# Optimization experiments

Measured on AMD Instinct MI355X. Metric: run time of the kernel, lower is better.

Reference implementation:

```python
import jax, jax.numpy as jnp
from jax import lax
import numpy as np

DN = ('NCHW', 'OIHW', 'NCHW')

def conv(x, w, b, stride, pad):
    y = lax.conv_general_dilated(x, w, (stride, stride), [(pad, pad), (pad, pad)], dimension_numbers=DN)
    return y if b is None else y + b[None, :, None, None]

def conv_transpose(x, w, b):
    # torch ConvTranspose2d(k=4, s=2, p=1); w in torch layout (Cin, Cout, 4, 4)
    w_f = jnp.flip(w, (2, 3)).transpose(1, 0, 2, 3)  # -> OIHW, flipped
    y = lax.conv_general_dilated(x, w_f, (1, 1), [(2, 2), (2, 2)], lhs_dilation=(2, 2), dimension_numbers=DN)
    return y + b[None, :, None, None]

def res_stack(x, w3, w1, n_layers=2):
    # shared weights across layers (ModuleList([layer]*n) aliases one module)
    for _ in range(n_layers):
        h = conv(jax.nn.relu(x), w3, None, 1, 1)
        h = conv(jax.nn.relu(h), w1, None, 1, 0)
        x = x + h
    return jax.nn.relu(x)

def setup_inputs() -> dict:
    key = jax.random.key(0)
    ks = jax.random.split(key, 16)
    s = 0.02
    d = {
        'x': jax.random.normal(ks[0], (32, 3, 256, 256), jnp.float32),
        'enc_w1': jax.random.normal(ks[1], (128, 3, 4, 4), jnp.float32) * s,
        'enc_b1': jnp.zeros((128,), jnp.float32),
        'enc_w2': jax.random.normal(ks[2], (256, 128, 4, 4), jnp.float32) * s,
        'enc_b2': jnp.zeros((256,), jnp.float32),
        'enc_w3': jax.random.normal(ks[3], (512, 256, 4, 4), jnp.float32) * s,
        'enc_b3': jnp.zeros((512,), jnp.float32),
        'enc_res_w3': jax.random.normal(ks[4], (32, 512, 3, 3), jnp.float32) * s,
        'enc_res_w1': jax.random.normal(ks[5], (512, 32, 1, 1), jnp.float32) * s,
        'prevq_w': jax.random.normal(ks[6], (64, 512, 1, 1), jnp.float32) * s,
        'prevq_b': jnp.zeros((64,), jnp.float32),
        'emb': jax.random.normal(ks[7], (512, 64), jnp.float32),
        'dec_w1': jax.random.normal(ks[8], (64, 256, 4, 4), jnp.float32) * s,
        'dec_b1': jnp.zeros((256,), jnp.float32),
        'dec_res_w3': jax.random.normal(ks[9], (32, 256, 3, 3), jnp.float32) * s,
        'dec_res_w1': jax.random.normal(ks[10], (256, 32, 1, 1), jnp.float32) * s,
        'dec_w2': jax.random.normal(ks[11], (256, 128, 4, 4), jnp.float32) * s,
        'dec_b2': jnp.zeros((128,), jnp.float32),
        'dec_w3': jax.random.normal(ks[12], (128, 3, 4, 4), jnp.float32) * s,
        'dec_b3': jnp.zeros((3,), jnp.float32),
    }
    return d

def vqvae_fwd(x, enc_w1, enc_b1, enc_w2, enc_b2, enc_w3, enc_b3, enc_res_w3, enc_res_w1,
              prevq_w, prevq_b, emb, dec_w1, dec_b1, dec_res_w3, dec_res_w1,
              dec_w2, dec_b2, dec_w3, dec_b3):
    # encoder
    z = jax.nn.relu(conv(x, enc_w1, enc_b1, 2, 1))
    z = jax.nn.relu(conv(z, enc_w2, enc_b2, 2, 1))
    z = conv(z, enc_w3, enc_b3, 2, 1)
    z = res_stack(z, enc_res_w3, enc_res_w1)
    z_e = conv(z, prevq_w, prevq_b, 1, 0)  # (B, D=64, 32, 32)
    # vector quantiser
    B, C, H, W = z_e.shape
    x_flat = z_e.reshape(B, C, H * W).transpose(0, 2, 1)  # (B, HW, D)
    d2 = (jnp.sum(x_flat ** 2, -1, keepdims=True)
          - 2.0 * jnp.einsum('bnd,kd->bnk', x_flat, emb)
          + jnp.sum(emb ** 2, -1))
    idx = jnp.argmin(d2, axis=2)  # (B, HW)
    z_q_flat = emb[idx]  # (B, HW, D)
    z_q = z_q_flat.transpose(0, 2, 1).reshape(B, C, H, W)
    sg = lax.stop_gradient
    q_loss = jnp.mean((sg(z_q_flat) - x_flat) ** 2) + jnp.mean((z_q_flat - sg(x_flat)) ** 2)
    # decoder
    y = conv_transpose(z_q, dec_w1, dec_b1)  # (B, 256, 64, 64)
    y = res_stack(y, dec_res_w3, dec_res_w1)
    y = jax.nn.relu(conv_transpose(y, dec_w2, dec_b2))
    y = conv_transpose(y, dec_w3, dec_b3)  # (B, 3, 256, 256)
    return y, q_loss

def reference(x, enc_w1, enc_b1, enc_w2, enc_b2, enc_w3, enc_b3, enc_res_w3, enc_res_w1,
              prevq_w, prevq_b, emb, dec_w1, dec_b1, dec_res_w3, dec_res_w1,
              dec_w2, dec_b2, dec_w3, dec_b3):
    return vqvae_fwd(x, enc_w1, enc_b1, enc_w2, enc_b2, enc_w3, enc_b3, enc_res_w3, enc_res_w1,
                     prevq_w, prevq_b, emb, dec_w1, dec_b1, dec_res_w3, dec_res_w1,
                     dec_w2, dec_b2, dec_w3, dec_b3)
```

## Files before the change

kernel.cpp:

```cpp
#include <hip/hip_runtime.h>
#include <hip/hip_bf16.h>

typedef __attribute__((ext_vector_type(8))) short short8;
typedef __attribute__((ext_vector_type(4))) float f32x4;
typedef __attribute__((ext_vector_type(4))) unsigned int uint4v;

__device__ __forceinline__ unsigned short f2bf(float f) {
  unsigned u = __builtin_bit_cast(unsigned, f);
  u = (u + 0x7FFFu + ((u >> 16) & 1u)) >> 16;
  return (unsigned short)u;
}
__device__ __forceinline__ float bf2f(unsigned short h) {
  unsigned u = ((unsigned)h) << 16;
  return __builtin_bit_cast(float, u);
}
__device__ __forceinline__ unsigned pk_bf16(float a, float b) {
  __hip_bfloat162 h = __float22bfloat162_rn(make_float2(a, b));
  unsigned u;
  __builtin_memcpy(&u, &h, 4);
  return u;
}

template<int TMT, int MT, int MODE, int ZSP, bool SPLIT, bool RELU_IN, bool RELU_OUT, bool BIAS, int SM>
__global__ __launch_bounds__(256, 4) void k_mfconv(
    const float* __restrict__ in, const unsigned short* __restrict__ wp,
    const float* __restrict__ bias, float* __restrict__ out,
    int Ci, int inW, int inH, int pWSH, int pHWSH,
    int Co, int ntap, int ntt,
    unsigned syp, unsigned sxp,
    int outW, int outHW, int CoSt) {
  const int tid  = threadIdx.x;
  const int lane = tid & 63, wave = tid >> 6;
  const int pW  = 1 << pWSH;
  const int pHW = 1 << pHWSH;
  const int inHW = inW * inH;
  const int nk32 = Ci >> 5;
  const int KS   = (nk32 >= 2) ? 2 : 1;
  const int NITS = 4 * KS;
  const int cpt  = nk32 / KS;
  const int total = ntap * cpt;
  constexpr int TT = TMT * MT;

  int bx = blockIdx.x;
  const int gx = gridDim.x;
  if ((gx & 7) == 0) bx = (bx & 7) * (gx >> 3) + (bx >> 3);
  const int n0  = bx * 64;
  const int coG = blockIdx.y;
  const int ph  = (MODE == 1) ? blockIdx.z : 0;
  const int tap0 = (MODE == 1) ? ph * 4 : 0;
  const int pdy = ph >> 1, pdx = ph & 1;

  int it0 = 0, itEnd = total;
  if (MODE != 1 && ZSP > 1) {
    const int per = total / ZSP;
    it0 = blockIdx.z * per;
    itEnd = it0 + per;
  }

  constexpr int NPL = SPLIT ? 2 : 1;
  constexpr int PL = 64 * 70;
  __shared__ __align__(16) unsigned short Bs[2 * NPL * PL];

  const int px  = lane;
  const int p   = n0 + px;
  const int img = p >> pHWSH;
  const int rem = p & (pHW - 1);
  const int y   = rem >> pWSH;
  const int x   = rem & (pW - 1);
  const size_t base_img = (size_t)img * Ci * inHW;

  constexpr int NTO = (TMT == 4) ? 4 : 2;
  const int mt0 = (TMT == 4) ? wave : (wave & 1);
  const int ntb = (TMT == 4) ? 0 : ((wave >> 1) * 2);
  f32x4 acc[MT * NTO];
#pragma unroll
  for (int u = 0; u < MT * NTO; ++u) acc[u] = (f32x4){0.f, 0.f, 0.f, 0.f};

  const int cp = wave;
  float v[16];

  auto ldr = [&](int tap_, int chunk_) {
    const int T = tap0 + tap_;
    const int dy = (int)((syp >> (2 * T)) & 3u) - 1;
    const int dx = (int)((sxp >> (2 * T)) & 3u) - 1;
    const int ys = (MODE == 2) ? (2 * y + dy) : (y + dy);
    const int xs = (MODE == 2) ? (2 * x + dx) : (x + dx);
    const bool ok = ((unsigned)ys < (unsigned)inH) && ((unsigned)xs < (unsigned)inW);
    const float* __restrict__ ipb = in + base_img + (ptrdiff_t)ys * inW + xs;
    const int ci0 = chunk_ * (KS * 32);
#pragma unroll
    for (int it2 = 0; it2 < 8; ++it2) {
      if (it2 >= NITS) break;
      const int cl = 2 * (cp + 4 * it2);
      float a = 0.f, b = 0.f;
      if (ok) {
        a = ipb[(size_t)(ci0 + cl) * inHW];
        b = ipb[(size_t)(ci0 + cl + 1) * inHW];
      }
      if (RELU_IN) { a = fmaxf(a, 0.f); b = fmaxf(b, 0.f); }
      v[2 * it2] = a; v[2 * it2 + 1] = b;
    }
  };
  auto pwr = [&](int b) {
#pragma unroll
    for (int it2 = 0; it2 < 8; ++it2) {
      if (it2 >= NITS) break;
      const int cl = 2 * (cp + 4 * it2);
      float a = v[2 * it2], c = v[2 * it2 + 1];
      unsigned hp = pk_bf16(a, c);
      *(unsigned*)&Bs[(b * NPL) * PL + px * 70 + cl] = hp;
      if (SPLIT) {
        float h0 = bf2f((unsigned short)hp), h1 = bf2f((unsigned short)(hp >> 16));
        *(unsigned*)&Bs[(b * NPL + 1) * PL + px * 70 + cl] = pk_bf16(a - h0, c - h1);
      }
    }
  };

  int tap = it0 / cpt, chunk = it0 % cpt;
  ldr(tap, chunk);
  pwr(0);
  __syncthreads();

  for (int it = it0; it < itEnd; ++it) {
    const int b = (it - it0) & 1;
    const int T = tap0 + tap;
    int tap2 = tap, chunk2 = chunk + 1;
    if (chunk2 == cpt) { chunk2 = 0; tap2 = tap + 1; }
    const bool more = (it + 1 < itEnd);
    if (more) ldr(tap2, chunk2);
#pragma unroll
    for (int s = 0; s < 2; ++s) {
      if (s >= KS) break;
      const int cic = chunk * KS + s;
      short8 ah[MT], al[MT];
#pragma unroll
      for (int m = 0; m < MT; ++m) {
        const int mtm = mt0 + m * TMT;
        size_t abase;
        if (SPLIT) abase = ((((size_t)coG * ntt + T) * nk32 + cic) * 2 * TT + mtm) * 512;
        else       abase = ((((size_t)coG * ntt + T) * nk32 + cic) * TT + mtm) * 512;
        ah[m] = *(const short8*)(wp + abase + (size_t)lane * 8);
        if (SPLIT) al[m] = *(const short8*)(wp + abase + (size_t)TT * 512 + (size_t)lane * 8);
      }
      short8 bh[NTO], bl[NTO];
#pragma unroll
      for (int u = 0; u < NTO; ++u) {
        const int row = 16 * (ntb + u) + (lane & 15);
        const unsigned* bp = (const unsigned*)&Bs[(b * NPL) * PL + row * 70 + s * 32 + (lane >> 4) * 8];
        uint4v hv = {bp[0], bp[1], bp[2], bp[3]};
        bh[u] = __builtin_bit_cast(short8, hv);
        if (SPLIT) {
          const unsigned* bpl = bp + (PL >> 1);
          uint4v lv = {bpl[0], bpl[1], bpl[2], bpl[3]};
          bl[u] = __builtin_bit_cast(short8, lv);
        }
      }
#pragma unroll
      for (int m = 0; m < MT; ++m)
#pragma unroll
        for (int u = 0; u < NTO; ++u) {
          f32x4 a = acc[m * NTO + u];
          a = __builtin_amdgcn_mfma_f32_16x16x32_bf16(ah[m], bh[u], a, 0, 0, 0);
          if (SPLIT) {
            a = __builtin_amdgcn_mfma_f32_16x16x32_bf16(al[m], bh[u], a, 0, 0, 0);
            a = __builtin_amdgcn_mfma_f32_16x16x32_bf16(ah[m], bl[u], a, 0, 0, 0);
          }
          acc[m * NTO + u] = a;
        }
    }
    if (more) {
      pwr(b ^ 1);
      __syncthreads();
    }
    tap = tap2; chunk = chunk2;
  }

#pragma unroll
  for (int m = 0; m < MT; ++m) {
    const int mtm = mt0 + m * TMT;
#pragma unroll
    for (int u = 0; u < NTO; ++u) {
      const int nt = ntb + u;
      const int pn = n0 + nt * 16 + (lane & 15);
      const int img2 = pn >> pHWSH;
      const int rem2 = pn & (pHW - 1);
      const int y2 = rem2 >> pWSH, x2 = rem2 & (pW - 1);
      int oy, ox;
      if (MODE == 1) { oy = 2 * y2 + pdy; ox = 2 * x2 + pdx; }
      else           { oy = y2;           ox = x2; }
#pragma unroll
      for (int r = 0; r < 4; ++r) {
        const int co = coG * (TT * 16) + mtm * 16 + (lane >> 4) * 4 + r;
        if (co < CoSt) {
          float val = acc[m * NTO + u][r];
          if (BIAS) val += bias[co];
          if (RELU_OUT) val = fmaxf(val, 0.f);
          size_t oi = ((size_t)img2 * Co + co) * outHW + (size_t)oy * outW + ox;
          if (SM == 0) out[oi] = val;
          else if (SM == 1) out[oi] += val;
          else atomicAdd(&out[oi], val);
        }
      }
    }
  }
}

__global__ __launch_bounds__(256, 4) void k_mfenc1(
    const float* __restrict__ in, const unsigned short* __restrict__ wp,
    const float* __restrict__ bias, float* __restrict__ out) {
  const int tid = threadIdx.x, lane = tid & 63, wave = tid >> 6;
  int bx = blockIdx.x;
  const int gx = gridDim.x;
  if ((gx & 7) == 0) bx = (bx & 7) * (gx >> 3) + (bx >> 3);
  const int n0 = bx * 64;
  const int p = n0 + lane;
  const int img = p >> 14;
  const int rem = p & 16383;
  const int y = rem >> 7, x = rem & 127;
  __shared__ __align__(16) unsigned short Bs[2 * 4480];
  const float* __restrict__ ib = in + (size_t)img * 3 * 65536;
#pragma unroll
  for (int i = 0; i < 8; ++i) {
    const int kk0 = 2 * (wave + 4 * i);
    float vv[2];
#pragma unroll
    for (int q = 0; q < 2; ++q) {
      const int kk = kk0 + q;
      const int tap = kk >> 2, c = kk & 3;
      const int iy = 2 * y + (tap >> 2) - 1, ix = 2 * x + (tap & 3) - 1;
      const bool ok = (c < 3) && ((unsigned)iy < 256u) && ((unsigned)ix < 256u);
      vv[q] = ok ? ib[((size_t)c << 16) + (size_t)iy * 256 + ix] : 0.f;
    }
    unsigned hp = pk_bf16(vv[0], vv[1]);
    *(unsigned*)&Bs[lane * 70 + kk0] = hp;
    float h0 = bf2f((unsigned short)hp), h1 = bf2f((unsigned short)(hp >> 16));
    *(unsigned*)&Bs[4480 + lane * 70 + kk0] = pk_bf16(vv[0] - h0, vv[1] - h1);
  }
  __syncthreads();

  f32x4 acc[8];
#pragma unroll
  for (int u = 0; u < 8; ++u) acc[u] = (f32x4){0.f, 0.f, 0.f, 0.f};
#pragma unroll
  for (int s = 0; s < 2; ++s) {
    short8 ah[2], al[2];
#pragma unroll
    for (int m = 0; m < 2; ++m) {
      const int mtm = wave + m * 4;
      size_t abase = (((size_t)s * 2 + 0) * 8 + mtm) * 512;
      ah[m] = *(const short8*)(wp + abase + (size_t)lane * 8);
      al[m] = *(const short8*)(wp + abase + 8 * 512 + (size_t)lane * 8);
    }
    short8 bh[4], bl[4];
#pragma unroll
    for (int u = 0; u < 4; ++u) {
      const int row = 16 * u + (lane & 15);
      const unsigned* bp = (const unsigned*)&Bs[row * 70 + s * 32 + (lane >> 4) * 8];
      uint4v hv = {bp[0], bp[1], bp[2], bp[3]};
      bh[u] = __builtin_bit_cast(short8, hv);
      const unsigned* bpl = bp + 2240;
      uint4v lv = {bpl[0], bpl[1], bpl[2], bpl[3]};
      bl[u] = __builtin_bit_cast(short8, lv);
    }
#pragma unroll
    for (int m = 0; m < 2; ++m)
#pragma unroll
      for (int u = 0; u < 4; ++u) {
        f32x4 a = acc[m * 4 + u];
        a = __builtin_amdgcn_mfma_f32_16x16x32_bf16(ah[m], bh[u], a, 0, 0, 0);
        a = __builtin_amdgcn_mfma_f32_16x16x32_bf16(al[m], bh[u], a, 0, 0, 0);
        a = __builtin_amdgcn_mfma_f32_16x16x32_bf16(ah[m], bl[u], a, 0, 0, 0);
        acc[m * 4 + u] = a;
      }
  }
#pragma unroll
  for (int m = 0; m < 2; ++m)
#pragma unroll
    for (int u = 0; u < 4; ++u) {
      const int pn = n0 + u * 16 + (lane & 15);
      const int img2 = pn >> 14;
      const int rem2 = pn & 16383;
#pragma unroll
      for (int r = 0; r < 4; ++r) {
        const int co = (wave + m * 4) * 16 + (lane >> 4) * 4 + r;
// ... 314 lines not shown
      e2  = fmaf(ev, ev, e2);
    }
    float score = e2 - 2.f * dot;
    if (score < best) { best = score; bi = k; }
  }
  const float* __restrict__ eb = emb + (size_t)bi * 64;
  float* __restrict__ qp = zq + (size_t)n * 64 * P + p;
  float l = 0.f;
#pragma unroll
  for (int d = 0; d < 64; ++d) {
    float ev = eb[d];
    qp[(size_t)d * P] = ev;
    float df = ev - xv[d];
    l = fmaf(df, df, l);
  }
#pragma unroll
  for (int off = 32; off > 0; off >>= 1) l += __shfl_down(l, off, 64);
  if ((threadIdx.x & 63) == 0) atomicAdd(loss, l * (2.f / 2097152.f));
}

extern "C" void kernel_launch(void* const* d_in, const int* in_sizes, int n_in,
                              void* d_out, int out_size, void* d_ws, size_t ws_size,
                              hipStream_t stream) {
  const float* x    = (const float*)d_in[0];
  const float* ew1  = (const float*)d_in[1];
  const float* eb1  = (const float*)d_in[2];
  const float* ew2  = (const float*)d_in[3];
  const float* eb2  = (const float*)d_in[4];
  const float* ew3  = (const float*)d_in[5];
  const float* eb3  = (const float*)d_in[6];
  const float* erw3 = (const float*)d_in[7];
  const float* erw1 = (const float*)d_in[8];
  const float* pqw  = (const float*)d_in[9];
  const float* pqb  = (const float*)d_in[10];
  const float* emb  = (const float*)d_in[11];
  const float* dw1  = (const float*)d_in[12];
  const float* db1  = (const float*)d_in[13];
  const float* drw3 = (const float*)d_in[14];
  const float* drw1 = (const float*)d_in[15];
  const float* dw2  = (const float*)d_in[16];
  const float* db2  = (const float*)d_in[17];
  const float* dw3  = (const float*)d_in[18];
  const float* db3  = (const float*)d_in[19];
  float* out = (float*)d_out;
  char*  ws  = (char*)d_ws;
  float* loss = out + 6291456;
  const size_t MiB = 1048576ull, KiB = 1024ull;

  dim3 blk(256);
  hipMemsetAsync(loss, 0, 4, stream);

  unsigned syct = 0, sxct = 0;
  for (int T = 0; T < 16; ++T) {
    int phx = T >> 2, dy = phx >> 1, dx = phx & 1, t = T & 3, ty = t >> 1, tx = t & 1;
    int sy = (dy == 0) ? (ty ? -1 : 0) : (ty ? 0 : 1);
    int sx = (dx == 0) ? (tx ? -1 : 0) : (tx ? 0 : 1);
    syct |= (unsigned)(sy + 1) << (2 * T);
    sxct |= (unsigned)(sx + 1) << (2 * T);
  }
  unsigned syc3 = 0, sxc3 = 0;
  for (int t = 0; t < 9; ++t) {
    syc3 |= (unsigned)(t / 3) << (2 * t);
    sxc3 |= (unsigned)(t % 3) << (2 * t);
  }
  unsigned syc4 = 0, sxc4 = 0;
  for (int t = 0; t < 16; ++t) {
    syc4 |= (unsigned)(t / 4) << (2 * t);
    sxc4 |= (unsigned)(t % 4) << (2 * t);
  }
  const unsigned sy1 = 1, sx1 = 1;

  auto packs = [&](char* PB) {
    unsigned short* e2p   = (unsigned short*)(PB);
    unsigned short* e3p   = (unsigned short*)(PB + 2048 * KiB);
    unsigned short* erc3p = (unsigned short*)(PB + 10240 * KiB);
    unsigned short* erc1p = (unsigned short*)(PB + 10816 * KiB);
    unsigned short* pqp   = (unsigned short*)(PB + 10880 * KiB);
    unsigned short* d1p   = (unsigned short*)(PB + 11008 * KiB);
    unsigned short* d2p   = (unsigned short*)(PB + 11520 * KiB);
    unsigned short* dc3p  = (unsigned short*)(PB + 12544 * KiB);
    unsigned short* dc1p  = (unsigned short*)(PB + 12688 * KiB);
    unsigned short* e1p   = (unsigned short*)(PB + 12704 * KiB);
    unsigned short* d3p   = (unsigned short*)(PB + 12832 * KiB);
    k_pack_o<true ><<<dim3(1048576 / 256), blk, 0, stream>>>(ew2,  e2p,  256, 128, 16, 8, 1048576);
    k_pack_o<true ><<<dim3(4194304 / 256), blk, 0, stream>>>(ew3,  e3p,  512, 256, 16, 8, 4194304);
    k_pack_o<true ><<<dim3(294912 / 256),  blk, 0, stream>>>(erw3, erc3p, 32, 512,  9, 2, 294912);
    k_pack_o<true ><<<dim3(32768 / 256),   blk, 0, stream>>>(erw1, erc1p, 512, 32,  1, 8, 32768);
    k_pack_o<true ><<<dim3(65536 / 256),   blk, 0, stream>>>(pqw,  pqp,   64, 512,  1, 4, 65536);
    k_pack_ct<<<dim3(262144 / 256), blk, 0, stream>>>(dw1, d1p, 64, 256, 8, 262144);
    k_pack_ct<<<dim3(524288 / 256), blk, 0, stream>>>(dw2, d2p, 256, 128, 8, 524288);
    k_pack_o<false><<<dim3(73728 / 256),   blk, 0, stream>>>(drw3, dc3p,  32, 256,  9, 2, 73728);
    k_pack_o<false><<<dim3(8192 / 256),    blk, 0, stream>>>(drw1, dc1p, 256, 32,  1, 8, 8192);
    k_pack_e1<<<dim3(256), blk, 0, stream>>>(ew1, e1p);
    k_pack_ct<<<dim3(65536 / 256), blk, 0, stream>>>(dw3, d3p, 128, 3, 2, 65536);
  };

  if (ws_size >= 498ull * MiB) {
    float* z1 = (float*)ws;
    float* z2 = (float*)(ws + 256 * MiB);
    float* z3 = (float*)(ws + 384 * MiB);
    float* h  = (float*)(ws + 448 * MiB);
    float* ze = (float*)(ws + 452 * MiB);
    float* zq = (float*)(ws + 460 * MiB);
    float* hd = (float*)(ws + 468 * MiB);
    char*  PB = ws + 484 * MiB;
    unsigned short* e2p   = (unsigned short*)(PB);
    unsigned short* e3p   = (unsigned short*)(PB + 2048 * KiB);
    unsigned short* erc3p = (unsigned short*)(PB + 10240 * KiB);
    unsigned short* erc1p = (unsigned short*)(PB + 10816 * KiB);
    unsigned short* pqp   = (unsigned short*)(PB + 10880 * KiB);
    unsigned short* d1p   = (unsigned short*)(PB + 11008 * KiB);
    unsigned short* d2p   = (unsigned short*)(PB + 11520 * KiB);
    unsigned short* dc3p  = (unsigned short*)(PB + 12544 * KiB);
    unsigned short* dc1p  = (unsigned short*)(PB + 12688 * KiB);
    unsigned short* e1p   = (unsigned short*)(PB + 12704 * KiB);
    unsigned short* d3p   = (unsigned short*)(PB + 12832 * KiB);
    packs(PB);

    k_mfenc1<<<dim3(8192), blk, 0, stream>>>(x, e1p, eb1, z1);
    k_mfconv<4, 2, 2, 1, true, false, true, true, 0><<<dim3(2048, 2), blk, 0, stream>>>(
        z1, e2p, eb2, z2, 128, 128, 128, 6, 12, 256, 16, 16, syc4, sxc4, 64, 4096, 256);
    k_mfconv<4, 2, 2, 1, true, false, false, true, 0><<<dim3(512, 4), blk, 0, stream>>>(
        z2, e3p, eb3, z3, 256, 64, 64, 5, 10, 512, 16, 16, syc4, sxc4, 32, 1024, 512);
    for (int i = 0; i < 2; ++i) {
      hipMemsetAsync(h, 0, 4 * MiB, stream);
      k_mfconv<2, 1, 0, 3, true, true, false, false, 2><<<dim3(512, 1, 3), blk, 0, stream>>>(
          z3, erc3p, nullptr, h, 512, 32, 32, 5, 10, 32, 9, 9, syc3, sxc3, 32, 1024, 32);
      k_mfconv<4, 2, 0, 1, true, true, false, false, 1><<<dim3(512, 4), blk, 0, stream>>>(
          h, erc1p, nullptr, z3, 32, 32, 32, 5, 10, 512, 1, 1, sy1, sx1, 32, 1024, 512);
    }
    hipMemsetAsync(ze, 0, 8 * MiB, stream);
    k_mfconv<4, 1, 0, 4, true, true, false, false, 2><<<dim3(512, 1, 4), blk, 0, stream>>>(
        z3, pqp, nullptr, ze, 512, 32, 32, 5, 10, 64, 1, 1, sy1, sx1, 32, 1024, 64);
    k_vq<<<dim3(128), blk, 0, stream>>>(ze, emb, pqb, zq, loss);
    float* y1 = (float*)(ws + 256 * MiB);
    float* y2 = (float*)ws;
    k_mfconv<4, 2, 1, 1, false, false, false, true, 0><<<dim3(512, 2, 4), blk, 0, stream>>>(
        zq, d1p, db1, y1, 64, 32, 32, 5, 10, 256, 4, 16, syct, sxct, 64, 4096, 256);
    for (int i = 0; i < 2; ++i) {
      hipMemsetAsync(hd, 0, 16 * MiB, stream);
      k_mfconv<2, 1, 0, 3, false, true, false, false, 2><<<dim3(2048, 1, 3), blk, 0, stream>>>(
          y1, dc3p, nullptr, hd, 256, 64, 64, 6, 12, 32, 9, 9, syc3, sxc3, 64, 4096, 32);
      k_mfconv<4, 2, 0, 1, false, true, false, false, 1><<<dim3(2048, 2), blk, 0, stream>>>(
          hd, dc1p, nullptr, y1, 32, 64, 64, 6, 12, 256, 1, 1, sy1, sx1, 64, 4096, 256);
    }
    k_mfconv<4, 2, 1, 1, false, true, true, true, 0><<<dim3(2048, 1, 4), blk, 0, stream>>>(
        y1, d2p, db2, y2, 256, 64, 64, 6, 12, 128, 4, 16, syct, sxct, 128, 16384, 128);
    k_mfconv<2, 1, 1, 1, false, false, false, true, 0><<<dim3(8192, 1, 4), blk, 0, stream>>>(
        y2, d3p, db3, out, 128, 128, 128, 7, 14, 3, 4, 16, syct, sxct, 256, 65536, 3);
    return;
  }

  if (ws_size >= 128ull * MiB) {
    float* z3  = (float*)ws;
    float* h   = (float*)(ws + 64 * MiB);
    float* ze  = (float*)(ws + 68 * MiB);
    float* zq  = (float*)(ws + 100 * MiB);
    char*  PB  = ws + 115 * MiB;
    unsigned short* e2p   = (unsigned short*)(PB);
    unsigned short* e3p   = (unsigned short*)(PB + 2048 * KiB);
    unsigned short* erc3p = (unsigned short*)(PB + 10240 * KiB);
    unsigned short* erc1p = (unsigned short*)(PB + 10816 * KiB);
    unsigned short* pqp   = (unsigned short*)(PB + 10880 * KiB);
    unsigned short* d1p   = (unsigned short*)(PB + 11008 * KiB);
    unsigned short* d2p   = (unsigned short*)(PB + 11520 * KiB);
    unsigned short* dc3p  = (unsigned short*)(PB + 12544 * KiB);
    unsigned short* dc1p  = (unsigned short*)(PB + 12688 * KiB);
    unsigned short* e1p   = (unsigned short*)(PB + 12704 * KiB);
    unsigned short* d3p   = (unsigned short*)(PB + 12832 * KiB);
    packs(PB);

    const int NE = 4;
    float* z1c = (float*)(ws + 64 * MiB);
    float* z2c = (float*)(ws + 96 * MiB);
    for (int n0 = 0; n0 < 32; n0 += NE) {
      const float* xb = x + (size_t)n0 * 3 * 65536;
      float* z3b = z3 + (size_t)n0 * 512 * 1024;
      k_mfenc1<<<dim3(NE * 256), blk, 0, stream>>>(xb, e1p, eb1, z1c);
      k_mfconv<4, 2, 2, 1, true, false, true, true, 0><<<dim3(256, 2), blk, 0, stream>>>(
          z1c, e2p, eb2, z2c, 128, 128, 128, 6, 12, 256, 16, 16, syc4, sxc4, 64, 4096, 256);
      k_mfconv<4, 2, 2, 1, true, false, false, true, 0><<<dim3(64, 4), blk, 0, stream>>>(
          z2c, e3p, eb3, z3b, 256, 64, 64, 5, 10, 512, 16, 16, syc4, sxc4, 32, 1024, 512);
    }
    for (int i = 0; i < 2; ++i) {
      hipMemsetAsync(h, 0, 4 * MiB, stream);
      k_mfconv<2, 1, 0, 3, true, true, false, false, 2><<<dim3(512, 1, 3), blk, 0, stream>>>(
          z3, erc3p, nullptr, h, 512, 32, 32, 5, 10, 32, 9, 9, syc3, sxc3, 32, 1024, 32);
      k_mfconv<4, 2, 0, 1, true, true, false, false, 1><<<dim3(512, 4), blk, 0, stream>>>(
          h, erc1p, nullptr, z3, 32, 32, 32, 5, 10, 512, 1, 1, sy1, sx1, 32, 1024, 512);
    }
    hipMemsetAsync(ze, 0, 8 * MiB, stream);
    k_mfconv<4, 1, 0, 4, true, true, false, false, 2><<<dim3(512, 1, 4), blk, 0, stream>>>(
        z3, pqp, nullptr, ze, 512, 32, 32, 5, 10, 64, 1, 1, sy1, sx1, 32, 1024, 64);
    k_vq<<<dim3(128), blk, 0, stream>>>(ze, emb, pqb, zq, loss);

    const int ND = 8;
    float* y1c = (float*)ws;
    float* hd  = (float*)(ws + 32 * MiB);
    float* y2c = (float*)(ws + 36 * MiB);
    for (int c = 0; c < 32; c += ND) {
      const float* zqb = zq + (size_t)c * 64 * 1024;
      float* outb = out + (size_t)c * 3 * 65536;
      k_mfconv<4, 2, 1, 1, false, false, false, true, 0><<<dim3(128, 2, 4), blk, 0, stream>>>(
          zqb, d1p, db1, y1c, 64, 32, 32, 5, 10, 256, 4, 16, syct, sxct, 64, 4096, 256);
      for (int i = 0; i < 2; ++i) {
        hipMemsetAsync(hd, 0, 4 * MiB, stream);
        k_mfconv<2, 1, 0, 3, false, true, false, false, 2><<<dim3(512, 1, 3), blk, 0, stream>>>(
            y1c, dc3p, nullptr, hd, 256, 64, 64, 6, 12, 32, 9, 9, syc3, sxc3, 64, 4096, 32);
        k_mfconv<4, 2, 0, 1, false, true, false, false, 1><<<dim3(512, 2), blk, 0, stream>>>(
            hd, dc1p, nullptr, y1c, 32, 64, 64, 6, 12, 256, 1, 1, sy1, sx1, 64, 4096, 256);
      }
      k_mfconv<4, 2, 1, 1, false, true, true, true, 0><<<dim3(512, 1, 4), blk, 0, stream>>>(
          y1c, d2p, db2, y2c, 256, 64, 64, 6, 12, 128, 4, 16, syct, sxct, 128, 16384, 128);
      k_mfconv<2, 1, 1, 1, false, false, false, true, 0><<<dim3(2048, 1, 4), blk, 0, stream>>>(
          y2c, d3p, db3, outb, 128, 128, 128, 7, 14, 3, 4, 16, syct, sxct, 256, 65536, 3);
    }
    return;
  }

  const size_t PER_IMG = 12582912ull;
  int NB = (int)(ws_size / PER_IMG);
  if (NB > 32) NB = 32;
  if (NB < 1)  NB = 1;

  for (int n0 = 0; n0 < 32; n0 += NB) {
    const int nb = (32 - n0 < NB) ? (32 - n0) : NB;
    const float* xb   = x   + (size_t)n0 * 3 * 65536;
    float*       outb = out + (size_t)n0 * 3 * 65536;

    float* z1 = (float*)ws;
    float* z2 = (float*)(ws + (size_t)NB * 8388608ull);
    float* z3 = (float*)ws;
    char*  tb = ws + (size_t)NB * 2097152ull;
    float* he = (float*)tb;
    float* ze = (float*)(tb + (size_t)NB * 131072ull);
    float* zq = (float*)(tb + (size_t)NB * 393216ull);
    float* hd = (float*)(tb + (size_t)NB * 655360ull);
    float* y1 = z2;
    float* y2 = (float*)ws;

    k_conv4<4, true ><<<dim3(8, 8, nb * 32), blk, 0, stream>>>(xb, ew1, eb1, z1, nb,   3, 256, 256, 128);
    k_conv4<4, true ><<<dim3(4, 4, nb * 64), blk, 0, stream>>>(z1, ew2, eb2, z2, nb, 128, 128, 128, 256);
    k_conv4<4, false><<<dim3(2, 2, nb * 128), blk, 0, stream>>>(z2, ew3, eb3, z3, nb, 256,  64,  64, 512);
    for (int i = 0; i < 2; ++i) {
      k_conv3<4, true, 1><<<dim3(2, 2, nb * 8), blk, 0, stream>>>(z3, erw3, he, nb, 512, 32, 32, 32);
      k_conv1<8, true, true><<<dim3(4, 64, nb), blk, 0, stream>>>(he, erw1, nullptr, z3, nb, 32, 1024, 512);
    }
    k_conv1<8, true, false><<<dim3(4, 8, nb), blk, 0, stream>>>(z3, pqw, pqb, ze, nb, 512, 1024, 64);
    k_vq64<<<dim3(nb * 16), dim3(64), 0, stream>>>(ze, emb, zq, loss, nb, 1024, 512);
    k_convT<4, false, false><<<dim3(2, 2, nb * 64), blk, 0, stream>>>(zq, dw1, db1, y1, nb,  64, 32, 32, 256);
    for (int i = 0; i < 2; ++i) {
      k_conv3<4, true, 1><<<dim3(4, 4, nb * 8), blk, 0, stream>>>(y1, drw3, hd, nb, 256, 64, 64, 32);
      k_conv1<8, true, true><<<dim3(16, 32, nb), blk, 0, stream>>>(hd, drw1, nullptr, y1, nb, 32, 4096, 256);
    }
    k_convT<4, true, true ><<<dim3(4, 4, nb * 32), blk, 0, stream>>>(y1, dw2, db2, y2, nb, 256, 64, 64, 128);
    k_convT<1, false, false><<<dim3(8, 8, nb * 3), blk, 0, stream>>>(y2, dw3, db3, outb, nb, 128, 128, 128, 3);
  }
}
```

Baseline: 4.172 ms.

## Add halo-tiled LDS conv kernel for 3x3 and transposed convs, drop split-K atomics

Adds a new kernel, k_mfhalo, that stages a spatial halo tile of 32 input channels in LDS once per channel chunk. All taps (9 for the 3x3, 16 for the transposed conv, covering all four output phases) read their MFMA B operands from that tile instead of re-gathering inputs from global memory per tap. The 3x3 residual convs no longer use split-K with atomicAdd and a preceding memset, and the transposed convs no longer launch one block per phase. The transposed-conv weight packing grouping changes to match. In exchange there is more LDS per block, no double buffering, and a larger accumulator per block for the transposed-conv path, which can lower occupancy.

```diff
diff --git a/kernel.cpp b/kernel.cpp
--- a/kernel.cpp
+++ b/kernel.cpp
@@ -19,6 +19,135 @@
   unsigned u;
   __builtin_memcpy(&u, &h, 4);
   return u;
+}
+
+template<int TMT, int CT, bool SPLIT, bool RELU_IN, bool RELU_OUT, bool BIAS>
+__global__ __launch_bounds__(256, (CT == 1) ? 2 : 4) void k_mfhalo(
+    const float* __restrict__ in, const unsigned short* __restrict__ wp,
+    const float* __restrict__ bias, float* __restrict__ out,
+    int Ci, int inW, int inH, int pWSH, int pHWSH,
+    int Co, int ntt, unsigned syp, unsigned sxp, int CoSt) {
+  constexpr int NTAP = (CT == 1) ? 16 : 9;
+  constexpr int NPH  = (CT == 1) ? 4 : 1;
+  constexpr int NTO  = (TMT == 4) ? 4 : 2;
+  constexpr int PLH  = 224 * 42;
+  const int tid = threadIdx.x, lane = tid & 63, wave = tid >> 6;
+
+  int bx = blockIdx.x;
+  const int gx = gridDim.x;
+  if ((gx & 7) == 0) bx = (bx & 7) * (gx >> 3) + (bx >> 3);
+  const int n0  = bx * 64;
+  const int coG = blockIdx.y;
+
+  const int pW  = 1 << pWSH;
+  const int pHW = 1 << pHWSH;
+  const int W = inW, H = inH;
+  const int inHW = W * H;
+  const int img  = n0 >> pHWSH;
+  const int rem0 = n0 & (pHW - 1);
+  const int y0   = rem0 >> pWSH;
+  const int x0   = rem0 & (pW - 1);
+  const int NR   = (pWSH >= 6) ? 1 : 2;
+  const int HWd  = ((pW < 64) ? pW : 64) + 2;
+  const int HROWS = (NR + 2) * HWd;
+  const int nk32 = Ci >> 5;
+  const size_t base_img = (size_t)img * Ci * inHW;
+
+  __shared__ __align__(16) unsigned short Hs[(SPLIT ? 2 : 1) * PLH];
+
+  const int mt  = (TMT == 4) ? wave : (wave & 1);
+  const int ntb = (TMT == 4) ? 0 : ((wave >> 1) * 2);
+  const int lsh = (pW < 64) ? pWSH : 6;
+  const int lxm = (pW < 64) ? (pW - 1) : 63;
+
+  f32x4 acc[NPH * NTO];
+#pragma unroll
+  for (int u = 0; u < NPH * NTO; ++u) acc[u] = (f32x4){0.f, 0.f, 0.f, 0.f};
+
+  const int srow0 = tid >> 4;
+  const int scl   = (tid & 15) * 2;
+
+  for (int cic = 0; cic < nk32; ++cic) {
+    if (cic) __syncthreads();
+    {
+      const int ci0 = cic * 32;
+      int hy = 0, hx = srow0;
+      for (int h = srow0; h < HROWS; h += 16) {
+        const int iy = y0 - 1 + hy;
+        const int ix = x0 - 1 + hx;
+        const bool ok = ((unsigned)iy < (unsigned)H) && ((unsigned)ix < (unsigned)W);
+        float a = 0.f, b = 0.f;
+        if (ok) {
+          const float* q = in + base_img + (size_t)(ci0 + scl) * inHW + (size_t)iy * W + ix;
+          a = q[0]; b = q[inHW];
+        }
+        if (RELU_IN) { a = fmaxf(a, 0.f); b = fmaxf(b, 0.f); }
+        unsigned hp = pk_bf16(a, b);
+        *(unsigned*)&Hs[h * 42 + scl] = hp;
+        if (SPLIT) {
+          float h0 = bf2f((unsigned short)hp), h1 = bf2f((unsigned short)(hp >> 16));
+          *(unsigned*)&Hs[PLH + h * 42 + scl] = pk_bf16(a - h0, b - h1);
+        }
+        hx += 16; if (hx >= HWd) { hx -= HWd; hy++; }
+      }
+    }
+    __syncthreads();
+#pragma unroll
+    for (int T = 0; T < NTAP; ++T) {
+      const int ency = (int)((syp >> (2 * T)) & 3u);
+      const int encx = (int)((sxp >> (2 * T)) & 3u);
+      size_t abase = (((size_t)coG * ntt + T) * nk32 + cic) * (SPLIT ? 2 : 1) * TMT * 512
+                     + (size_t)mt * 512;
+      short8 ah = *(const short8*)(wp + abase + (size_t)lane * 8);
+      short8 al;
+      if (SPLIT) al = *(const short8*)(wp + abase + (size_t)TMT * 512 + (size_t)lane * 8);
+      const int ph = (CT == 1) ? (T >> 2) : 0;
+#pragma unroll
+      for (int u = 0; u < NTO; ++u) {
+        const int pnl = (ntb + u) * 16 + (lane & 15);
+        const int ly = pnl >> lsh, lx = pnl & lxm;
+        const int h = (ly + ency) * HWd + lx + encx;
+        const unsigned* bp = (const unsigned*)&Hs[h * 42 + (lane >> 4) * 8];
+        uint4v hv = {bp[0], bp[1], bp[2], bp[3]};
+        short8 bh = __builtin_bit_cast(short8, hv);
+        f32x4 a = acc[ph * NTO + u];
+        a = __builtin_amdgcn_mfma_f32_16x16x32_bf16(ah, bh, a, 0, 0, 0);
+        if (SPLIT) {
+          const unsigned* bpl = bp + (PLH >> 1);
+          uint4v lv = {bpl[0], bpl[1], bpl[2], bpl[3]};
+          short8 bl = __builtin_bit_cast(short8, lv);
+          a = __builtin_amdgcn_mfma_f32_16x16x32_bf16(al, bh, a, 0, 0, 0);
+          a = __builtin_amdgcn_mfma_f32_16x16x32_bf16(ah, bl, a, 0, 0, 0);
+        }
+        acc[ph * NTO + u] = a;
+      }
+    }
+  }
+
+  const int outW  = (CT == 1) ? 2 * pW : pW;
+  const int outHW = (CT == 1) ? 4 * pHW : pHW;
+#pragma unroll
+  for (int u = 0; u < NTO; ++u) {
+    const int pn = n0 + (ntb + u) * 16 + (lane & 15);
+    const int rem2 = pn & (pHW - 1);
+    const int y2 = rem2 >> pWSH, x2 = rem2 & (pW - 1);
+#pragma unroll
+    for (int ph = 0; ph < NPH; ++ph) {
+      int oy, ox;
+      if (CT == 1) { oy = 2 * y2 + (ph >> 1); ox = 2 * x2 + (ph & 1); }
+      else         { oy = y2;                 ox = x2; }
+#pragma unroll
+      for (int r = 0; r < 4; ++r) {
+        const int co = coG * (TMT * 16) + mt * 16 + (lane >> 4) * 4 + r;
+        if (co < CoSt) {
+          float val = acc[ph * NTO + u][r];
+          if (BIAS) val += bias[co];
+          if (RELU_OUT) val = fmaxf(val, 0.f);
+          out[((size_t)img * Co + co) * outHW + (size_t)oy * outW + ox] = val;
+        }
+      }
+    }
+  }
 }
 
 template<int TMT, int MT, int MODE, int ZSP, bool SPLIT, bool RELU_IN, bool RELU_OUT, bool BIAS, int SM>
@@ -46,12 +175,9 @@
   if ((gx & 7) == 0) bx = (bx & 7) * (gx >> 3) + (bx >> 3);
   const int n0  = bx * 64;
   const int coG = blockIdx.y;
-  const int ph  = (MODE == 1) ? blockIdx.z : 0;
-  const int tap0 = (MODE == 1) ? ph * 4 : 0;
-  const int pdy = ph >> 1, pdx = ph & 1;
 
   int it0 = 0, itEnd = total;
-  if (MODE != 1 && ZSP > 1) {
+  if (ZSP > 1) {
     const int per = total / ZSP;
     it0 = blockIdx.z * per;
     itEnd = it0 + per;
@@ -80,7 +206,7 @@
   float v[16];
 
   auto ldr = [&](int tap_, int chunk_) {
-    const int T = tap0 + tap_;
+    const int T = tap_;
     const int dy = (int)((syp >> (2 * T)) & 3u) - 1;
     const int dx = (int)((sxp >> (2 * T)) & 3u) - 1;
     const int ys = (MODE == 2) ? (2 * y + dy) : (y + dy);
@@ -123,7 +249,7 @@
 
   for (int it = it0; it < itEnd; ++it) {
     const int b = (it - it0) & 1;
-    const int T = tap0 + tap;
+    const int T = tap;
     int tap2 = tap, chunk2 = chunk + 1;
     if (chunk2 == cpt) { chunk2 = 0; tap2 = tap + 1; }
     const bool more = (it + 1 < itEnd);
@@ -185,9 +311,6 @@
       const int img2 = pn >> pHWSH;
       const int rem2 = pn & (pHW - 1);
       const int y2 = rem2 >> pWSH, x2 = rem2 & (pW - 1);
-      int oy, ox;
-      if (MODE == 1) { oy = 2 * y2 + pdy; ox = 2 * x2 + pdx; }
-      else           { oy = y2;           ox = x2; }
 #pragma unroll
       for (int r = 0; r < 4; ++r) {
         const int co = coG * (TT * 16) + mtm * 16 + (lane >> 4) * 4 + r;
@@ -195,7 +318,7 @@
           float val = acc[m * NTO + u][r];
           if (BIAS) val += bias[co];
           if (RELU_OUT) val = fmaxf(val, 0.f);
-          size_t oi = ((size_t)img2 * Co + co) * outHW + (size_t)oy * outW + ox;
+          size_t oi = ((size_t)img2 * Co + co) * outHW + (size_t)y2 * outW + x2;
           if (SM == 0) out[oi] = val;
           else if (SM == 1) out[oi] += val;
           else atomicAdd(&out[oi], val);
@@ -685,8 +808,8 @@
     k_pack_o<true ><<<dim3(294912 / 256),  blk, 0, stream>>>(erw3, erc3p, 32, 512,  9, 2, 294912);
     k_pack_o<true ><<<dim3(32768 / 256),   blk, 0, stream>>>(erw1, erc1p, 512, 32,  1, 8, 32768);
     k_pack_o<true ><<<dim3(65536 / 256),   blk, 0, stream>>>(pqw,  pqp,   64, 512,  1, 4, 65536);
-    k_pack_ct<<<dim3(262144 / 256), blk, 0, stream>>>(dw1, d1p, 64, 256, 8, 262144);
-    k_pack_ct<<<dim3(524288 / 256), blk, 0, stream>>>(dw2, d2p, 256, 128, 8, 524288);
+    k_pack_ct<<<dim3(262144 / 256), blk, 0, stream>>>(dw1, d1p, 64, 256, 4, 262144);
+    k_pack_ct<<<dim3(524288 / 256), blk, 0, stream>>>(dw2, d2p, 256, 128, 4, 524288);
     k_pack_o<false><<<dim3(73728 / 256),   blk, 0, stream>>>(drw3, dc3p,  32, 256,  9, 2, 73728);
     k_pack_o<false><<<dim3(8192 / 256),    blk, 0, stream>>>(drw1, dc1p, 256, 32,  1, 8, 8192);
     k_pack_e1<<<dim3(256), blk, 0, stream>>>(ew1, e1p);
@@ -721,9 +844,8 @@
     k_mfconv<4, 2, 2, 1, true, false, false, true, 0><<<dim3(512, 4), blk, 0, stream>>>(
         z2, e3p, eb3, z3, 256, 64, 64, 5, 10, 512, 16, 16, syc4, sxc4, 32, 1024, 512);
     for (int i = 0; i < 2; ++i) {
-      hipMemsetAsync(h, 0, 4 * MiB, stream);
-      k_mfconv<2, 1, 0, 3, true, true, false, false, 2><<<dim3(512, 1, 3), blk, 0, stream>>>(
-          z3, erc3p, nullptr, h, 512, 32, 32, 5, 10, 32, 9, 9, syc3, sxc3, 32, 1024, 32);
+      k_mfhalo<2, 0, true, true, false, false><<<dim3(512, 1), blk, 0, stream>>>(
+          z3, erc3p, nullptr, h, 512, 32, 32, 5, 10, 32, 9, syc3, sxc3, 32);
       k_mfconv<4, 2, 0, 1, true, true, false, false, 1><<<dim3(512, 4), blk, 0, stream>>>(
           h, erc1p, nullptr, z3, 32, 32, 32, 5, 10, 512, 1, 1, sy1, sx1, 32, 1024, 512);
     }
@@ -733,19 +855,18 @@
     k_vq<<<dim3(128), blk, 0, stream>>>(ze, emb, pqb, zq, loss);
     float* y1 = (float*)(ws + 256 * MiB);
     float* y2 = (float*)ws;
-    k_mfconv<4, 2, 1, 1, false, false, false, true, 0><<<dim3(512, 2, 4), blk, 0, stream>>>(
-        zq, d1p, db1, y1, 64, 32, 32, 5, 10, 256, 4, 16, syct, sxct, 64, 4096, 256);
+    k_mfhalo<4, 1, false, false, false, true><<<dim3(512, 4), blk, 0, stream>>>(
+        zq, d1p, db1, y1, 64, 32, 32, 5, 10, 256, 16, syct, sxct, 256);
     for (int i = 0; i < 2; ++i) {
-      hipMemsetAsync(hd, 0, 16 * MiB, stream);
-      k_mfconv<2, 1, 0, 3, false, true, false, false, 2><<<dim3(2048, 1, 3), blk, 0, stream>>>(
-          y1, dc3p, nullptr, hd, 256, 64, 64, 6, 12, 32, 9, 9, syc3, sxc3, 64, 4096, 32);
+      k_mfhalo<2, 0, false, true, false, false><<<dim3(2048, 1), blk, 0, stream>>>(
+          y1, dc3p, nullptr, hd, 256, 64, 64, 6, 12, 32, 9, syc3, sxc3, 32);
       k_mfconv<4, 2, 0, 1, false, true, false, false, 1><<<dim3(2048, 2), blk, 0, stream>>>(
           hd, dc1p, nullptr, y1, 32, 64, 64, 6, 12, 256, 1, 1, sy1, sx1, 64, 4096, 256);
     }
-    k_mfconv<4, 2, 1, 1, false, true, true, true, 0><<<dim3(2048, 1, 4), blk, 0, stream>>>(
-        y1, d2p, db2, y2, 256, 64, 64, 6, 12, 128, 4, 16, syct, sxct, 128, 16384, 128);
-    k_mfconv<2, 1, 1, 1, false, false, false, true, 0><<<dim3(8192, 1, 4), blk, 0, stream>>>(
-        y2, d3p, db3, out, 128, 128, 128, 7, 14, 3, 4, 16, syct, sxct, 256, 65536, 3);
+    k_mfhalo<4, 1, false, true, true, true><<<dim3(2048, 2), blk, 0, stream>>>(
+        y1, d2p, db2, y2, 256, 64, 64, 6, 12, 128, 16, syct, sxct, 128);
+    k_mfhalo<2, 1, false, false, false, true><<<dim3(8192, 1), blk, 0, stream>>>(
+        y2, d3p, db3, out, 128, 128, 128, 7, 14, 3, 16, syct, sxct, 3);
     return;
   }
 
@@ -781,9 +902,8 @@
           z2c, e3p, eb3, z3b, 256, 64, 64, 5, 10, 512, 16, 16, syc4, sxc4, 32, 1024, 512);
     }
     for (int i = 0; i < 2; ++i) {
-      hipMemsetAsync(h, 0, 4 * MiB, stream);
-      k_mfconv<2, 1, 0, 3, true, true, false, false, 2><<<dim3(512, 1, 3), blk, 0, stream>>>(
-          z3, erc3p, nullptr, h, 512, 32, 32, 5, 10, 32, 9, 9, syc3, sxc3, 32, 1024, 32);
+      k_mfhalo<2, 0, true, true, false, false><<<dim3(512, 1), blk, 0, stream>>>(
+          z3, erc3p, nullptr, h, 512, 32, 32, 5, 10, 32, 9, syc3, sxc3, 32);
       k_mfconv<4, 2, 0, 1, true, true, false, false, 1><<<dim3(512, 4), blk, 0, stream>>>(
           h, erc1p, nullptr, z3, 32, 32, 32, 5, 10, 512, 1, 1, sy1, sx1, 32, 1024, 512);
     }
@@ -799,19 +919,18 @@
     for (int c = 0; c < 32; c += ND) {
       const float* zqb = zq + (size_t)c * 64 * 1024;
       float* outb = out + (size_t)c * 3 * 65536;
-      k_mfconv<4, 2, 1, 1, false, false, false, true, 0><<<dim3(128, 2, 4), blk, 0, stream>>>(
-          zqb, d1p, db1, y1c, 64, 32, 32, 5, 10, 256, 4, 16, syct, sxct, 64, 4096, 256);
+      k_mfhalo<4, 1, false, false, false, true><<<dim3(128, 4), blk, 0, stream>>>(
+          zqb, d1p, db1, y1c, 64, 32, 32, 5, 10, 256, 16, syct, sxct, 256);
       for (int i = 0; i < 2; ++i) {
-        hipMemsetAsync(hd, 0, 4 * MiB, stream);
-        k_mfconv<2, 1, 0, 3, false, true, false, false, 2><<<dim3(512, 1, 3), blk, 0, stream>>>(
-            y1c, dc3p, nullptr, hd, 256, 64, 64, 6, 12, 32, 9, 9, syc3, sxc3, 64, 4096, 32);
+        k_mfhalo<2, 0, false, true, false, false><<<dim3(512, 1), blk, 0, stream>>>(
+            y1c, dc3p, nullptr, hd, 256, 64, 64, 6, 12, 32, 9, syc3, sxc3, 32);
         k_mfconv<4, 2, 0, 1, false, true, false, false, 1><<<dim3(512, 2), blk, 0, stream>>>(
             hd, dc1p, nullptr, y1c, 32, 64, 64, 6, 12, 256, 1, 1, sy1, sx1, 64, 4096, 256);
       }
-      k_mfconv<4, 2, 1, 1, false, true, true, true, 0><<<dim3(512, 1, 4), blk, 0, stream>>>(
-          y1c, d2p, db2, y2c, 256, 64, 64, 6, 12, 128, 4, 16, syct, sxct, 128, 16384, 128);
-      k_mfconv<2, 1, 1, 1, false, false, false, true, 0><<<dim3(2048, 1, 4), blk, 0, stream>>>(
-          y2c, d3p, db3, outb, 128, 128, 128, 7, 14, 3, 4, 16, syct, sxct, 256, 65536, 3);
+      k_mfhalo<4, 1, false, true, true, true><<<dim3(512, 2), blk, 0, stream>>>(
+          y1c, d2p, db2, y2c, 256, 64, 64, 6, 12, 128, 16, syct, sxct, 128);
+      k_mfhalo<2, 1, false, false, false, true><<<dim3(2048, 1), blk, 0, stream>>>(
+          y2c, d3p, db3, outb, 128, 128, 128, 7, 14, 3, 16, syct, sxct, 3);
     }
     return;
   }
```

After: 4.240 ms. Within noise of the previous version (+1.6%).

## Fuse residual 3x3 and 1x1 convolutions into one kernel per layer

Applied to the files above, without the earlier changes.

Adds k_mfres, which computes relu->3x3 conv (to 32 channels)->relu->1x1 conv->residual add in a single kernel. The hidden activation stays in shared memory instead of global memory, which removes the memset, the split-K atomic adds and the separate 1x1 pass. The kernel ping-pongs between two buffers so it does not write in place. In exchange, each block now covers all 9 taps and all input channels serially, which lowers parallelism compared with the split-K launches. It also needs new weight packings and adds shared-memory pressure.

```diff
diff --git a/kernel.cpp b/kernel.cpp
--- a/kernel.cpp
+++ b/kernel.cpp
@@ -200,6 +200,173 @@
           else if (SM == 1) out[oi] += val;
           else atomicAdd(&out[oi], val);
         }
+      }
+    }
+  }
+}
+
+template<int MGRP, bool SPLIT>
+__global__ __launch_bounds__(256, SPLIT ? 3 : 4) void k_mfres(
+    const float* __restrict__ in, const unsigned short* __restrict__ w3p,
+    const unsigned short* __restrict__ w1p, float* __restrict__ znew,
+    int pWSH, int pHWSH, unsigned syp, unsigned sxp) {
+  constexpr int C = MGRP * 64;
+  const int tid = threadIdx.x, lane = tid & 63, wave = tid >> 6;
+  const int pW = 1 << pWSH, pHW = 1 << pHWSH;
+  const int inW = pW, inH = pHW >> pWSH;
+  const int inHW = pHW;
+  const int nk32 = C >> 5;
+  const int cpt = nk32 >> 1;
+  const int total = 9 * cpt;
+
+  int bx = blockIdx.x;
+  const int gx = gridDim.x;
+  if ((gx & 7) == 0) bx = (bx & 7) * (gx >> 3) + (bx >> 3);
+  const int n0 = bx * 64;
+
+  constexpr int NPL = SPLIT ? 2 : 1;
+  constexpr int PL = 64 * 70;
+  __shared__ __align__(16) unsigned short Bs[2 * NPL * PL];
+  __shared__ __align__(16) unsigned short Hs2[NPL * 2560];
+
+  const int px = lane;
+  const int p = n0 + px;
+  const int img = p >> pHWSH;
+  const int rem = p & (pHW - 1);
+  const int y = rem >> pWSH, x = rem & (pW - 1);
+  const size_t base_img = (size_t)img * C * inHW;
+  const int mt = wave & 1, ntb = (wave >> 1) * 2;
+  const int cp = wave;
+  float v[16];
+  f32x4 acc[2];
+  acc[0] = (f32x4){0.f, 0.f, 0.f, 0.f};
+  acc[1] = (f32x4){0.f, 0.f, 0.f, 0.f};
+
+  auto ldr = [&](int T, int chunk_) {
+    const int dy = (int)((syp >> (2 * T)) & 3u) - 1;
+    const int dx = (int)((sxp >> (2 * T)) & 3u) - 1;
+    const int ys = y + dy, xs = x + dx;
+    const bool ok = ((unsigned)ys < (unsigned)inH) && ((unsigned)xs < (unsigned)inW);
+    const float* __restrict__ ipb = in + base_img + (ptrdiff_t)ys * inW + xs;
+    const int ci0 = chunk_ * 64;
+#pragma unroll
+    for (int i2 = 0; i2 < 8; ++i2) {
+      const int cl = 2 * (cp + 4 * i2);
+      float a = 0.f, b = 0.f;
+      if (ok) {
+        a = ipb[(size_t)(ci0 + cl) * inHW];
+        b = ipb[(size_t)(ci0 + cl + 1) * inHW];
+      }
+      a = fmaxf(a, 0.f); b = fmaxf(b, 0.f);
+      v[2 * i2] = a; v[2 * i2 + 1] = b;
+    }
+  };
+  auto pwr = [&](int b) {
+#pragma unroll
+    for (int i2 = 0; i2 < 8; ++i2) {
+      const int cl = 2 * (cp + 4 * i2);
+      float a = v[2 * i2], c = v[2 * i2 + 1];
+      unsigned hp = pk_bf16(a, c);
+      *(unsigned*)&Bs[(b * NPL) * PL + px * 70 + cl] = hp;
+      if (SPLIT) {
+        float h0 = bf2f((unsigned short)hp), h1 = bf2f((unsigned short)(hp >> 16));
+        *(unsigned*)&Bs[(b * NPL + 1) * PL + px * 70 + cl] = pk_bf16(a - h0, c - h1);
+      }
+    }
+  };
+
+  int tap = 0, chunk = 0;
+  ldr(0, 0);
+  pwr(0);
+  __syncthreads();
+  for (int it = 0; it < total; ++it) {
+    const int b = it & 1;
+    const int T = tap;
+    int tap2 = tap, chunk2 = chunk + 1;
+    if (chunk2 == cpt) { chunk2 = 0; tap2 = tap + 1; }
+    const bool more = (it + 1 < total);
+    if (more) ldr(tap2, chunk2);
+#pragma unroll
+    for (int s = 0; s < 2; ++s) {
+      const int cic = chunk * 2 + s;
+      size_t abase;
+      if (SPLIT) abase = (((size_t)T * nk32 + cic) * 2 * 2 + mt) * 512;
+      else       abase = (((size_t)T * nk32 + cic) * 2 + mt) * 512;
+      short8 ah = *(const short8*)(w3p + abase + (size_t)lane * 8);
+      short8 al;
+      if (SPLIT) al = *(const short8*)(w3p + abase + 2 * 512 + (size_t)lane * 8);
+#pragma unroll
+      for (int u = 0; u < 2; ++u) {
+        const int row = 16 * (ntb + u) + (lane & 15);
+        const unsigned* bp = (const unsigned*)&Bs[(b * NPL) * PL + row * 70 + s * 32 + (lane >> 4) * 8];
+        uint4v hv = {bp[0], bp[1], bp[2], bp[3]};
+        short8 bh = __builtin_bit_cast(short8, hv);
+        f32x4 a = acc[u];
+        a = __builtin_amdgcn_mfma_f32_16x16x32_bf16(ah, bh, a, 0, 0, 0);
+        if (SPLIT) {
+          const unsigned* bpl = bp + (PL >> 1);
+          uint4v lv = {bpl[0], bpl[1], bpl[2], bpl[3]};
+          short8 bl = __builtin_bit_cast(short8, lv);
+          a = __builtin_amdgcn_mfma_f32_16x16x32_bf16(al, bh, a, 0, 0, 0);
+          a = __builtin_amdgcn_mfma_f32_16x16x32_bf16(ah, bl, a, 0, 0, 0);
+        }
+        acc[u] = a;
+      }
+    }
+    if (more) {
+      pwr(b ^ 1);
+      __syncthreads();
+    }
+    tap = tap2; chunk = chunk2;
+  }
+
+#pragma unroll
+  for (int u = 0; u < 2; ++u) {
+    const int pxl = (ntb + u) * 16 + (lane & 15);
+#pragma unroll
+    for (int r = 0; r < 4; ++r) {
+      const int co = mt * 16 + (lane >> 4) * 4 + r;
+      float val = fmaxf(acc[u][r], 0.f);
+      unsigned short hv = f2bf(val);
+      Hs2[pxl * 40 + co] = hv;
+      if (SPLIT) Hs2[2560 + pxl * 40 + co] = f2bf(val - bf2f(hv));
+    }
+  }
+  __syncthreads();
+
+  short8 bh2[4], bl2[4];
+#pragma unroll
+  for (int u = 0; u < 4; ++u) {
+    const int row = 16 * u + (lane & 15);
+    bh2[u] = *(const short8*)&Hs2[row * 40 + (lane >> 4) * 8];
+    if (SPLIT) bl2[u] = *(const short8*)&Hs2[2560 + row * 40 + (lane >> 4) * 8];
+  }
+#pragma unroll
+  for (int g = 0; g < MGRP; ++g) {
+    const int mt2 = wave + 4 * g;
+    short8 a1h = *(const short8*)(w1p + (size_t)mt2 * 512 + (size_t)lane * 8);
+    short8 a1l;
+    if (SPLIT) a1l = *(const short8*)(w1p + ((size_t)(MGRP * 4) + mt2) * 512 + (size_t)lane * 8);
+    f32x4 a2[4];
+#pragma unroll
+    for (int u = 0; u < 4; ++u) a2[u] = (f32x4){0.f, 0.f, 0.f, 0.f};
+#pragma unroll
+    for (int u = 0; u < 4; ++u) {
+      a2[u] = __builtin_amdgcn_mfma_f32_16x16x32_bf16(a1h, bh2[u], a2[u], 0, 0, 0);
+      if (SPLIT) {
+        a2[u] = __builtin_amdgcn_mfma_f32_16x16x32_bf16(a1l, bh2[u], a2[u], 0, 0, 0);
+        a2[u] = __builtin_amdgcn_mfma_f32_16x16x32_bf16(a1h, bl2[u], a2[u], 0, 0, 0);
+      }
+    }
+#pragma unroll
+    for (int u = 0; u < 4; ++u) {
+      const int pn = n0 + u * 16 + (lane & 15);
+      const int rem2 = pn & (pHW - 1);
+#pragma unroll
+      for (int r = 0; r < 4; ++r) {
+        const int co = mt2 * 16 + (lane >> 4) * 4 + r;
+        size_t oi = ((size_t)img * C + co) * inHW + rem2;
+        znew[oi] = in[oi] + a2[u][r];
       }
     }
   }
@@ -680,6 +847,8 @@
     unsigned short* dc1p  = (unsigned short*)(PB + 12688 * KiB);
     unsigned short* e1p   = (unsigned short*)(PB + 12704 * KiB);
     unsigned short* d3p   = (unsigned short*)(PB + 12832 * KiB);
+    unsigned short* erc1F = (unsigned short*)(PB + 12960 * KiB);
+    unsigned short* dc1F  = (unsigned short*)(PB + 13024 * KiB);
     k_pack_o<true ><<<dim3(1048576 / 256), blk, 0, stream>>>(ew2,  e2p,  256, 128, 16, 8, 1048576);
     k_pack_o<true ><<<dim3(4194304 / 256), blk, 0, stream>>>(ew3,  e3p,  512, 256, 16, 8, 4194304);
     k_pack_o<true ><<<dim3(294912 / 256),  blk, 0, stream>>>(erw3, erc3p, 32, 512,  9, 2, 294912);
@@ -691,28 +860,29 @@
     k_pack_o<false><<<dim3(8192 / 256),    blk, 0, stream>>>(drw1, dc1p, 256, 32,  1, 8, 8192);
     k_pack_e1<<<dim3(256), blk, 0, stream>>>(ew1, e1p);
     k_pack_ct<<<dim3(65536 / 256), blk, 0, stream>>>(dw3, d3p, 128, 3, 2, 65536);
+    k_pack_o<true ><<<dim3(32768 / 256), blk, 0, stream>>>(erw1, erc1F, 512, 32, 1, 32, 32768);
+    k_pack_o<false><<<dim3(8192 / 256),  blk, 0, stream>>>(drw1, dc1F, 256, 32, 1, 16, 8192);
   };
 
   if (ws_size >= 498ull * MiB) {
-    float* z1 = (float*)ws;
-    float* z2 = (float*)(ws + 256 * MiB);
-    float* z3 = (float*)(ws + 384 * MiB);
-    float* h  = (float*)(ws + 448 * MiB);
-    float* ze = (float*)(ws + 452 * MiB);
-    float* zq = (float*)(ws + 460 * MiB);
-    float* hd = (float*)(ws + 468 * MiB);
-    char*  PB = ws + 484 * MiB;
+    float* z1  = (float*)ws;
+    float* z2  = (float*)(ws + 256 * MiB);
+    float* z3  = (float*)(ws + 384 * MiB);
+    float* z3b = (float*)ws;
+    float* ze  = (float*)(ws + 452 * MiB);
+    float* zq  = (float*)(ws + 460 * MiB);
+    char*  PB  = ws + 484 * MiB;
     unsigned short* e2p   = (unsigned short*)(PB);
     unsigned short* e3p   = (unsigned short*)(PB + 2048 * KiB);
     unsigned short* erc3p = (unsigned short*)(PB + 10240 * KiB);
-    unsigned short* erc1p = (unsigned short*)(PB + 10816 * KiB);
     unsigned short* pqp   = (unsigned short*)(PB + 10880 * KiB);
     unsigned short* d1p   = (unsigned short*)(PB + 11008 * KiB);
     unsigned short* d2p   = (unsigned short*)(PB + 11520 * KiB);
     unsigned short* dc3p  = (unsigned short*)(PB + 12544 * KiB);
-    unsigned short* dc1p  = (unsigned short*)(PB + 12688 * KiB);
     unsigned short* e1p   = (unsigned short*)(PB + 12704 * KiB);
     unsigned short* d3p   = (unsigned short*)(PB + 12832 * KiB);
+    unsigned short* erc1F = (unsigned short*)(PB + 12960 * KiB);
+    unsigned short* dc1F  = (unsigned short*)(PB + 13024 * KiB);
     packs(PB);
 
     k_mfenc1<<<dim3(8192), blk, 0, stream>>>(x, e1p, eb1, z1);
@@ -720,28 +890,19 @@
         z1, e2p, eb2, z2, 128, 128, 128, 6, 12, 256, 16, 16, syc4, sxc4, 64, 4096, 256);
     k_mfconv<4, 2, 2, 1, true, false, false, true, 0><<<dim3(512, 4), blk, 0, stream>>>(
         z2, e3p, eb3, z3, 256, 64, 64, 5, 10, 512, 16, 16, syc4, sxc4, 32, 1024, 512);
-    for (int i = 0; i < 2; ++i) {
-      hipMemsetAsync(h, 0, 4 * MiB, stream);
-      k_mfconv<2, 1, 0, 3, true, true, false, false, 2><<<dim3(512, 1, 3), blk, 0, stream>>>(
-          z3, erc3p, nullptr, h, 512, 32, 32, 5, 10, 32, 9, 9, syc3, sxc3, 32, 1024, 32);
-      k_mfconv<4, 2, 0, 1, true, true, false, false, 1><<<dim3(512, 4), blk, 0, stream>>>(
-          h, erc1p, nullptr, z3, 32, 32, 32, 5, 10, 512, 1, 1, sy1, sx1, 32, 1024, 512);
-    }
+    k_mfres<8, true><<<dim3(512), blk, 0, stream>>>(z3,  erc3p, erc1F, z3b, 5, 10, syc3, sxc3);
+    k_mfres<8, true><<<dim3(512), blk, 0, stream>>>(z3b, erc3p, erc1F, z3,  5, 10, syc3, sxc3);
     hipMemsetAsync(ze, 0, 8 * MiB, stream);
     k_mfconv<4, 1, 0, 4, true, true, false, false, 2><<<dim3(512, 1, 4), blk, 0, stream>>>(
         z3, pqp, nullptr, ze, 512, 32, 32, 5, 10, 64, 1, 1, sy1, sx1, 32, 1024, 64);
     k_vq<<<dim3(128), blk, 0, stream>>>(ze, emb, pqb, zq, loss);
-    float* y1 = (float*)(ws + 256 * MiB);
-    float* y2 = (float*)ws;
+    float* y1  = (float*)(ws + 256 * MiB);
+    float* y1b = (float*)ws;
+    float* y2  = (float*)ws;
     k_mfconv<4, 2, 1, 1, false, false, false, true, 0><<<dim3(512, 2, 4), blk, 0, stream>>>(
         zq, d1p, db1, y1, 64, 32, 32, 5, 10, 256, 4, 16, syct, sxct, 64, 4096, 256);
-    for (int i = 0; i < 2; ++i) {
-      hipMemsetAsync(hd, 0, 16 * MiB, stream);
-      k_mfconv<2, 1, 0, 3, false, true, false, false, 2><<<dim3(2048, 1, 3), blk, 0, stream>>>(
-          y1, dc3p, nullptr, hd, 256, 64, 64, 6, 12, 32, 9, 9, syc3, sxc3, 64, 4096, 32);
-      k_mfconv<4, 2, 0, 1, false, true, false, false, 1><<<dim3(2048, 2), blk, 0, stream>>>(
-          hd, dc1p, nullptr, y1, 32, 64, 64, 6, 12, 256, 1, 1, sy1, sx1, 64, 4096, 256);
-    }
+    k_mfres<4, false><<<dim3(2048), blk, 0, stream>>>(y1,  dc3p, dc1F, y1b, 6, 12, syc3, sxc3);
+    k_mfres<4, false><<<dim3(2048), blk, 0, stream>>>(y1b, dc3p, dc1F, y1,  6, 12, syc3, sxc3);
     k_mfconv<4, 2, 1, 1, false, true, true, true, 0><<<dim3(2048, 1, 4), blk, 0, stream>>>(
         y1, d2p, db2, y2, 256, 64, 64, 6, 12, 128, 4, 16, syct, sxct, 128, 16384, 128);
     k_mfconv<2, 1, 1, 1, false, false, false, true, 0><<<dim3(8192, 1, 4), blk, 0, stream>>>(
@@ -773,12 +934,12 @@
     float* z2c = (float*)(ws + 96 * MiB);
     for (int n0 = 0; n0 < 32; n0 += NE) {
       const float* xb = x + (size_t)n0 * 3 * 65536;
-      float* z3b = z3 + (size_t)n0 * 512 * 1024;
+      float* z3b2 = z3 + (size_t)n0 * 512 * 1024;
       k_mfenc1<<<dim3(NE * 256), blk, 0, stream>>>(xb, e1p, eb1, z1c);
       k_mfconv<4, 2, 2, 1, true, false, true, true, 0><<<dim3(256, 2), blk, 0, stream>>>(
           z1c, e2p, eb2, z2c, 128, 128, 128, 6, 12, 256, 16, 16, syc4, sxc4, 64, 4096, 256);
       k_mfconv<4, 2, 2, 1, true, false, false, true, 0><<<dim3(64, 4), blk, 0, stream>>>(
-          z2c, e3p, eb3, z3b, 256, 64, 64, 5, 10, 512, 16, 16, syc4, sxc4, 32, 1024, 512);
+          z2c, e3p, eb3, z3b2, 256, 64, 64, 5, 10, 512, 16, 16, syc4, sxc4, 32, 1024, 512);
     }
     for (int i = 0; i < 2; ++i) {
       hipMemsetAsync(h, 0, 4 * MiB, stream);
```

Result: no change. 4.128 ms (-1.1%).
